# Kernel optimization log

Hardware: AMD Instinct MI355X
Metric: run time of the kernel (lower is better)

Reference implementation:

```python
import jax, jax.numpy as jnp
import numpy as np

N_NODES = 50000
N_EDGES = 819200  # divisible by num_rels=8 -> equal relation segments (implicit rel_ptr)
NUM_RELS = 8
N_HEADS = 4
IN_FEAT = 256
OUT_FEAT = 128
HEAD_DIM = OUT_FEAT // N_HEADS
LEAKY_SLOPE = 0.2


def setup_inputs() -> dict:
    key = jax.random.key(0)
    ks = jax.random.split(key, 7)
    inputs = jax.random.normal(ks[0], (N_NODES, IN_FEAT), dtype=jnp.float32)
    conv_weights = jax.random.normal(ks[1], (NUM_RELS, N_HEADS, IN_FEAT, HEAD_DIM), dtype=jnp.float32) * (1.0 / np.sqrt(IN_FEAT))
    attn_l = jax.random.normal(ks[2], (NUM_RELS, N_HEADS, HEAD_DIM), dtype=jnp.float32) * 0.1
    attn_r = jax.random.normal(ks[3], (NUM_RELS, N_HEADS, HEAD_DIM), dtype=jnp.float32) * 0.1
    h_bias = jax.random.normal(ks[4], (OUT_FEAT,), dtype=jnp.float32) * 0.01
    row_idx = jax.random.randint(ks[5], (N_EDGES,), 0, N_NODES, dtype=jnp.int32)
    col_idx = jax.random.randint(ks[6], (N_EDGES,), 0, N_NODES, dtype=jnp.int32)
    return {
        'inputs': inputs,
        'conv_weights': conv_weights,
        'attn_l': attn_l,
        'attn_r': attn_r,
        'h_bias': h_bias,
        'row_idx': row_idx,
        'col_idx': col_idx,
    }


def reference(inputs, conv_weights, attn_l, attn_r, h_bias, row_idx, col_idx):
    R, H, IN, D = conv_weights.shape
    E = row_idx.shape[0]
    N = inputs.shape[0]
    epr = E // R  # edges per relation (equal segments == rel_ptr)

    # relation-grouped GEMM: per-edge transformed src features [R, epr, H, D]
    src = inputs[row_idx].reshape(R, epr, IN)
    feat_src = jnp.einsum('rei,rhid->rehd', src, conv_weights)
    el = jnp.einsum('rehd,rhd->reh', feat_src, attn_l)

    dst = inputs[col_idx].reshape(R, epr, IN)
    feat_dst = jnp.einsum('rei,rhid->rehd', dst, conv_weights)
    er = jnp.einsum('rehd,rhd->reh', feat_dst, attn_r)

    # fused GAT: leaky_relu(el+er), softmax over incoming edges per dst node
    e = jax.nn.leaky_relu((el + er).reshape(E, H), negative_slope=LEAKY_SLOPE)
    m = jax.ops.segment_max(e, col_idx, num_segments=N)          # [N, H]
    e_exp = jnp.exp(e - m[col_idx])                              # [E, H]
    denom = jax.ops.segment_sum(e_exp, col_idx, num_segments=N)  # [N, H]
    alpha = e_exp / denom[col_idx]                               # [E, H]

    feat = feat_src.reshape(E, H, D)
    h = jax.ops.segment_sum(alpha[:, :, None] * feat, col_idx, num_segments=N)  # [N, H, D]
    h = h.reshape(N, H * D) + h_bias
    # activation=None, self_loop=False, dropout treated as eval (identity)
    return h
```

## Files before the change

### kernel.cpp

```cpp
#include <hip/hip_runtime.h>
#include <hip/hip_bf16.h>

#define N_NODES 50000
#define N_EDGES 819200
#define NUM_RELS 8
#define EPR (N_EDGES / NUM_RELS)
#define N_HEADS 4
#define IN_FEAT 256
#define OUT_FEAT 128
#define HEAD_DIM 32
#define NB_SCAN ((N_NODES + 255) / 256)

typedef __attribute__((ext_vector_type(8))) __bf16 bf16x8;
typedef __attribute__((ext_vector_type(4))) __bf16 bf16x4;
typedef __attribute__((ext_vector_type(4))) float f32x4;

#define SZ_FEAT ((size_t)NUM_RELS * N_NODES * OUT_FEAT)
#define SZ_EL ((size_t)NUM_RELS * N_NODES * N_HEADS)
#define SZ_WB ((size_t)IN_FEAT * 64)
#define SZ_WT ((size_t)NUM_RELS * OUT_FEAT * IN_FEAT / 2)
#define OFF_FEAT ((size_t)0)
#define OFF_EL (OFF_FEAT + SZ_FEAT)
#define OFF_ER (OFF_EL + SZ_EL)
#define OFF_WB (OFF_ER + SZ_EL)
#define OFF_WT (OFF_WB + SZ_WB)
#define OFF_INT (OFF_WT + SZ_WT)
#define IOFF_CNT ((size_t)0)
#define IOFF_PTR ((size_t)N_NODES)
#define IOFF_CUR ((size_t)2 * N_NODES)
#define IOFF_BSUM ((size_t)3 * N_NODES)
#define IOFF_SPAY ((size_t)3 * N_NODES + 256)

__global__ void k_wboth(const float* __restrict__ cw, const float* __restrict__ al,
                        const float* __restrict__ ar, __bf16* __restrict__ wbt) {
    int tid = blockIdx.x * blockDim.x + threadIdx.x;
    if (tid >= IN_FEAT * 64) return;
    int col = tid >> 8, i = tid & 255;
    int side = col >> 5, r = (col >> 2) & 7, h = col & 3;
    const float* av = (side ? ar : al) + (size_t)(r * N_HEADS + h) * HEAD_DIM;
    const float* cwp = cw + ((size_t)(r * N_HEADS + h) * IN_FEAT + i) * HEAD_DIM;
    float s = 0.f;
#pragma unroll
    for (int d = 0; d < HEAD_DIM; ++d) s += cwp[d] * av[d];
    wbt[(size_t)col * IN_FEAT + i] = (__bf16)s;
}

__global__ void k_cvt_w(const float* __restrict__ cw, __bf16* __restrict__ wt) {
    int tid = blockIdx.x * blockDim.x + threadIdx.x;
    if (tid >= NUM_RELS * N_HEADS * IN_FEAT * HEAD_DIM) return;
    int d = tid & 31, k = (tid >> 5) & 255, h = (tid >> 13) & 3, r = tid >> 15;
    float v = cw[tid];
    wt[((size_t)(r * OUT_FEAT + h * HEAD_DIM + d)) * IN_FEAT + k] = (__bf16)v;
}

__global__ __launch_bounds__(256) void k_fused(const float* __restrict__ x,
                                               const __bf16* __restrict__ wt,
                                               const __bf16* __restrict__ wbt,
                                               __bf16* __restrict__ featb,
                                               float* __restrict__ el,
                                               float* __restrict__ er) {
    __shared__ __align__(16) unsigned char sA[65536];
    __shared__ __align__(16) unsigned char sB[16384];
    const int t = threadIdx.x;
    const int lane = t & 63;
    const int w = t >> 6;
    const int wr = w >> 1, wc = w & 1;
    const int n0 = blockIdx.x * 128;

#pragma unroll 8
    for (int i = 0; i < 32; ++i) {
        int flat = i * 256 + t;
        int row = flat >> 6;
        int kq = flat & 63;
        int n = n0 + row;
        if (n >= N_NODES) n = N_NODES - 1;
        float4 v = *(const float4*)(x + (size_t)n * IN_FEAT + kq * 4);
        bf16x4 hv;
        hv[0] = (__bf16)v.x; hv[1] = (__bf16)v.y; hv[2] = (__bf16)v.z; hv[3] = (__bf16)v.w;
        int sg = kq >> 1;
        int slot = (sg & ~7) | ((sg & 7) ^ (row & 7));
        *(bf16x4*)(sA + row * 512 + slot * 16 + (kq & 1) * 8) = hv;
    }
    __syncthreads();

    f32x4 acc[4][4];

    for (int r = 0; r < NUM_RELS; ++r) {
#pragma unroll
        for (int i = 0; i < 4; ++i)
#pragma unroll
            for (int j = 0; j < 4; ++j) acc[i][j] = (f32x4){0.f, 0.f, 0.f, 0.f};
        const __bf16* wtr = wt + (size_t)r * OUT_FEAT * IN_FEAT;

        for (int kc = 0; kc < 4; ++kc) {
#pragma unroll
            for (int i = 0; i < 4; ++i) {
                int flat = i * 256 + t;
                int brow = flat >> 3;
                int s = flat & 7;
                int ssrc = s ^ (brow & 7);
                bf16x8 v = *(const bf16x8*)(wtr + (size_t)brow * IN_FEAT + kc * 64 + ssrc * 8);
                *(bf16x8*)(sB + brow * 128 + s * 16) = v;
            }
            __syncthreads();
#pragma unroll
            for (int ks = 0; ks < 2; ++ks) {
                bf16x8 af[4], bg[4];
#pragma unroll
                for (int rb = 0; rb < 4; ++rb) {
                    int row = wr * 64 + rb * 16 + (lane & 15);
                    int slot = kc * 8 + ((ks * 4 + (lane >> 4)) ^ (row & 7));
                    af[rb] = *(const bf16x8*)(sA + row * 512 + slot * 16);
                }
#pragma unroll
                for (int cb = 0; cb < 4; ++cb) {
                    int brow = wc * 64 + cb * 16 + (lane & 15);
                    int slot = (ks * 4 + (lane >> 4)) ^ (brow & 7);
                    bg[cb] = *(const bf16x8*)(sB + brow * 128 + slot * 16);
                }
#pragma unroll
                for (int rb = 0; rb < 4; ++rb)
#pragma unroll
                    for (int cb = 0; cb < 4; ++cb)
                        acc[rb][cb] = __builtin_amdgcn_mfma_f32_16x16x32_bf16(af[rb], bg[cb], acc[rb][cb], 0, 0, 0);
            }
            __syncthreads();
        }
#pragma unroll
        for (int rb = 0; rb < 4; ++rb) {
#pragma unroll
            for (int q = 0; q < 4; ++q) {
                int row = wr * 64 + rb * 16 + (lane >> 4) * 4 + q;
                int n = n0 + row;
                if (n < N_NODES) {
                    __bf16* fp = featb + ((size_t)r * N_NODES + n) * OUT_FEAT + wc * 64 + (lane & 15);
#pragma unroll
                    for (int cb = 0; cb < 4; ++cb) fp[cb * 16] = (__bf16)acc[rb][cb][q];
                }
            }
        }
    }

#pragma unroll
    for (int i = 0; i < 4; ++i)
#pragma unroll
        for (int j = 0; j < 2; ++j) acc[i][j] = (f32x4){0.f, 0.f, 0.f, 0.f};

    for (int kc = 0; kc < 4; ++kc) {
#pragma unroll
        for (int i = 0; i < 2; ++i) {
            int flat = i * 256 + t;
            int brow = flat >> 3;
            int s = flat & 7;
            int ssrc = s ^ (brow & 7);
            bf16x8 v = *(const bf16x8*)(wbt + (size_t)brow * IN_FEAT + kc * 64 + ssrc * 8);
            *(bf16x8*)(sB + brow * 128 + s * 16) = v;
        }
        __syncthreads();
#pragma unroll
        for (int ks = 0; ks < 2; ++ks) {
            bf16x8 af[4], bg[2];
#pragma unroll
            for (int rb = 0; rb < 4; ++rb) {
                int row = wr * 64 + rb * 16 + (lane & 15);
                int slot = kc * 8 + ((ks * 4 + (lane >> 4)) ^ (row & 7));
                af[rb] = *(const bf16x8*)(sA + row * 512 + slot * 16);
            }
#pragma unroll
            for (int cb = 0; cb < 2; ++cb) {
                int brow = wc * 32 + cb * 16 + (lane & 15);
                int slot = (ks * 4 + (lane >> 4)) ^ (brow & 7);
                bg[cb] = *(const bf16x8*)(sB + brow * 128 + slot * 16);
            }
#pragma unroll
            for (int rb = 0; rb < 4; ++rb)
#pragma unroll
                for (int cb = 0; cb < 2; ++cb)
                    acc[rb][cb] = __builtin_amdgcn_mfma_f32_16x16x32_bf16(af[rb], bg[cb], acc[rb][cb], 0, 0, 0);
        }
        __syncthreads();
    }
#pragma unroll
    for (int rb = 0; rb < 4; ++rb) {
#pragma unroll
        for (int q = 0; q < 4; ++q) {
            int n = n0 + wr * 64 + rb * 16 + (lane >> 4) * 4 + q;
            if (n < N_NODES) {
#pragma unroll
                for (int cb = 0; cb < 2; ++cb) {
                    int c = wc * 32 + cb * 16 + (lane & 15);
                    int side = c >> 5, rr = (c >> 2) & 7, h = c & 3;
                    float* dst = side ? er : el;
                    dst[((size_t)rr * N_NODES + n) * N_HEADS + h] = acc[rb][cb][q];
                }
            }
        }
    }
}

__global__ void k_hist(const int* __restrict__ col, int* __restrict__ cnt) {
    int e = blockIdx.x * blockDim.x + threadIdx.x;
    if (e < N_EDGES) atomicAdd(cnt + col[e], 1);
}

__global__ __launch_bounds__(256) void k_scanA(const int* __restrict__ cnt,
                                               int* __restrict__ excl,
                                               int* __restrict__ bsum) {
    __shared__ int s[256];
    int i = blockIdx.x * 256 + threadIdx.x;
    int v = (i < N_NODES) ? cnt[i] : 0;
    s[threadIdx.x] = v;
    __syncthreads();
#pragma unroll
    for (int off = 1; off < 256; off <<= 1) {
        int t = (threadIdx.x >= off) ? s[threadIdx.x - off] : 0;
        __syncthreads();
        s[threadIdx.x] += t;
        __syncthreads();
    }
    if (i < N_NODES) excl[i] = s[threadIdx.x] - v;
    if (threadIdx.x == 255) bsum[blockIdx.x] = s[255];
}

__global__ __launch_bounds__(256) void k_scanB(int* __restrict__ bsum) {
    __shared__ int s[256];
    int v = (threadIdx.x < NB_SCAN) ? bsum[threadIdx.x] : 0;
    s[threadIdx.x] = v;
    __syncthreads();
#pragma unroll
    for (int off = 1; off < 256; off <<= 1) {
        int t = (threadIdx.x >= off) ? s[threadIdx.x - off] : 0;
        __syncthreads();
        s[threadIdx.x] += t;
        __syncthreads();
    }
    bsum[threadIdx.x] = s[threadIdx.x] - v;
}

__global__ __launch_bounds__(256) void k_scanC(int* __restrict__ ptr,
                                               int* __restrict__ cursor,
                                               const int* __restrict__ bsum) {
    int i = blockIdx.x * 256 + threadIdx.x;
    if (i >= N_NODES) return;
    int p = ptr[i] + bsum[blockIdx.x];
    ptr[i] = p;
    cursor[i] = p;
}

__global__ void k_scatter(const int* __restrict__ row, const int* __restrict__ col,
                          int* __restrict__ cursor, int* __restrict__ spay) {
    int e = blockIdx.x * blockDim.x + threadIdx.x;
    if (e >= N_EDGES) return;
    int c = col[e];
    int pos = atomicAdd(cursor + c, 1);
    spay[pos] = row[e] | ((e / EPR) << 20);
}

__global__ __launch_bounds__(256) void k_agg(const int* __restrict__ ptr,
                                             const int* __restrict__ cnt,
                                             const int* __restrict__ spay,
                                             const float* __restrict__ el,
                                             const float* __restrict__ er,
                                             const __bf16* __restrict__ featb,
                                             const float* __restrict__ bias,
                                             float* __restrict__ out) {
    const int wv = threadIdx.x >> 6, lane = threadIdx.x & 63;
    const int n = blockIdx.x * 4 + wv;
    if (n >= N_NODES) return;
    const int start = ptr[n], len = cnt[n];
    const int h = lane >> 4;
    float accx = 0.f, accy = 0.f, den = 0.f;
    int j = 0;
    for (; j + 4 <= len; j += 4) {
        int p[4];
#pragma unroll
        for (int u = 0; u < 4; ++u) p[u] = spay[start + j + u];
        float w[4], vx[4], vy[4];
#pragma unroll
        for (int u = 0; u < 4; ++u) {
            int rw = p[u] & 0xFFFFF, r = p[u] >> 20;
            size_t rb = (size_t)r * N_NODES;
            float s = el[(rb + rw) * N_HEADS + h] + er[(rb + n) * N_HEADS + h];
            s = s > 0.f ? s : 0.2f * s;
            w[u] = __expf(s);
            ushort2 raw = *(const ushort2*)(featb + (rb + rw) * OUT_FEAT + lane * 2);
            vx[u] = __uint_as_float((unsigned)raw.x << 16);
            vy[u] = __uint_as_float((unsigned)raw.y << 16);
        }
#pragma unroll
        for (int u = 0; u < 4; ++u) {
            accx += w[u] * vx[u];
            accy += w[u] * vy[u];
            den += w[u];
        }
    }
    for (; j < len; ++j) {
        int p = spay[start + j];
        int rw = p & 0xFFFFF, r = p >> 20;
        size_t rb = (size_t)r * N_NODES;
        float s = el[(rb + rw) * N_HEADS + h] + er[(rb + n) * N_HEADS + h];
        s = s > 0.f ? s : 0.2f * s;
        float w = __expf(s);
        ushort2 raw = *(const ushort2*)(featb + (rb + rw) * OUT_FEAT + lane * 2);
        accx += w * __uint_as_float((unsigned)raw.x << 16);
        accy += w * __uint_as_float((unsigned)raw.y << 16);
        den += w;
    }
    float inv = (len > 0) ? 1.f / den : 0.f;
    int o = lane * 2;
    float2 res;
    res.x = accx * inv + bias[o];
    res.y = accy * inv + bias[o + 1];
    *(float2*)(out + (size_t)n * OUT_FEAT + o) = res;
}

extern "C" void kernel_launch(void* const* d_in, const int* in_sizes, int n_in,
                              void* d_out, int out_size, void* d_ws, size_t ws_size,
                              hipStream_t stream) {
    const float* x = (const float*)d_in[0];
    const float* cw = (const float*)d_in[1];
    const float* al = (const float*)d_in[2];
    const float* ar = (const float*)d_in[3];
    const float* bias = (const float*)d_in[4];
    const int* row = (const int*)d_in[5];
    const int* col = (const int*)d_in[6];
    float* out = (float*)d_out;
    float* ws = (float*)d_ws;

    __bf16* featb = (__bf16*)(ws + OFF_FEAT);
    float* el = ws + OFF_EL;
    float* er = ws + OFF_ER;
    __bf16* wbt = (__bf16*)(ws + OFF_WB);
    __bf16* wt = (__bf16*)(ws + OFF_WT);
    int* iw = (int*)(ws + OFF_INT);
    int* cnt = iw + IOFF_CNT;
    int* ptr = iw + IOFF_PTR;
    int* cur = iw + IOFF_CUR;
    int* bsum = iw + IOFF_BSUM;
    int* spay = iw + IOFF_SPAY;

    hipMemsetAsync(cnt, 0, N_NODES * sizeof(int), stream);

    k_wboth<<<(IN_FEAT * 64 + 255) / 256, 256, 0, stream>>>(cw, al, ar, wbt);
    k_cvt_w<<<(NUM_RELS * N_HEADS * IN_FEAT * HEAD_DIM + 255) / 256, 256, 0, stream>>>(cw, wt);
    k_fused<<<(N_NODES + 127) / 128, 256, 0, stream>>>(x, wt, wbt, featb, el, er);

    k_hist<<<(N_EDGES + 255) / 256, 256, 0, stream>>>(col, cnt);
    k_scanA<<<NB_SCAN, 256, 0, stream>>>(cnt, ptr, bsum);
    k_scanB<<<1, 256, 0, stream>>>(bsum);
    k_scanC<<<NB_SCAN, 256, 0, stream>>>(ptr, cur, bsum);
    k_scatter<<<(N_EDGES + 255) / 256, 256, 0, stream>>>(row, col, cur, spay);

    k_agg<<<(N_NODES + 3) / 4, 256, 0, stream>>>(ptr, cnt, spay, el, er, featb, bias, out);
}
```

Measured before the change: 213.4 us.

## Split wavefront into two half-waves processing alternate edges with 8-byte loads

The aggregation kernel now has each half of a 64-lane wavefront handle alternate incoming edges. Each lane loads four bf16 features (8 bytes) instead of two, and the two halves are combined with a cross-lane shuffle at the end. The per-relation er values for the destination node are preloaded into registers, so the loop no longer reloads them for every edge. This aims to double the number of independent gathers in flight per wave and widen each load, at the cost of predicated tail handling, an extra register array and a reduction step.

New measurement: 238.7 us. 1.12x slower.

```diff
diff --git a/kernel.cpp b/kernel.cpp
--- a/kernel.cpp
+++ b/kernel.cpp
@@ -268,50 +268,49 @@
     const int n = blockIdx.x * 4 + wv;
     if (n >= N_NODES) return;
     const int start = ptr[n], len = cnt[n];
-    const int h = lane >> 4;
-    float accx = 0.f, accy = 0.f, den = 0.f;
-    int j = 0;
-    for (; j + 4 <= len; j += 4) {
-        int p[4];
-#pragma unroll
-        for (int u = 0; u < 4; ++u) p[u] = spay[start + j + u];
-        float w[4], vx[4], vy[4];
-#pragma unroll
-        for (int u = 0; u < 4; ++u) {
-            int rw = p[u] & 0xFFFFF, r = p[u] >> 20;
-            size_t rb = (size_t)r * N_NODES;
-            float s = el[(rb + rw) * N_HEADS + h] + er[(rb + n) * N_HEADS + h];
-            s = s > 0.f ? s : 0.2f * s;
-            w[u] = __expf(s);
-            ushort2 raw = *(const ushort2*)(featb + (rb + rw) * OUT_FEAT + lane * 2);
-            vx[u] = __uint_as_float((unsigned)raw.x << 16);
-            vy[u] = __uint_as_float((unsigned)raw.y << 16);
-        }
-#pragma unroll
-        for (int u = 0; u < 4; ++u) {
-            accx += w[u] * vx[u];
-            accy += w[u] * vy[u];
-            den += w[u];
-        }
-    }
-    for (; j < len; ++j) {
-        int p = spay[start + j];
+    const int half = lane >> 5;
+    const int hl = lane & 31;
+    const int o0 = hl * 4;
+    const int h = o0 >> 5;
+
+    float er_r[8];
+#pragma unroll
+    for (int r = 0; r < 8; ++r)
+        er_r[r] = er[((size_t)r * N_NODES + n) * N_HEADS + h];
+
+    float a0 = 0.f, a1 = 0.f, a2 = 0.f, a3 = 0.f, den = 0.f;
+    const int nit = (len + 1) >> 1;
+#pragma unroll 2
+    for (int j = 0; j < nit; ++j) {
+        int idx = 2 * j + half;
+        bool valid = idx < len;
+        int p = valid ? spay[start + idx] : 0;
         int rw = p & 0xFFFFF, r = p >> 20;
         size_t rb = (size_t)r * N_NODES;
-        float s = el[(rb + rw) * N_HEADS + h] + er[(rb + n) * N_HEADS + h];
+        float s = el[(rb + rw) * N_HEADS + h] + er_r[r];
         s = s > 0.f ? s : 0.2f * s;
-        float w = __expf(s);
-        ushort2 raw = *(const ushort2*)(featb + (rb + rw) * OUT_FEAT + lane * 2);
-        accx += w * __uint_as_float((unsigned)raw.x << 16);
-        accy += w * __uint_as_float((unsigned)raw.y << 16);
-        den += w;
-    }
-    float inv = (len > 0) ? 1.f / den : 0.f;
-    int o = lane * 2;
-    float2 res;
-    res.x = accx * inv + bias[o];
-    res.y = accy * inv + bias[o + 1];
-    *(float2*)(out + (size_t)n * OUT_FEAT + o) = res;
+        float wgt = valid ? __expf(s) : 0.f;
+        ushort4 raw = *(const ushort4*)(featb + (rb + rw) * OUT_FEAT + o0);
+        a0 += wgt * __uint_as_float((unsigned)raw.x << 16);
+        a1 += wgt * __uint_as_float((unsigned)raw.y << 16);
+        a2 += wgt * __uint_as_float((unsigned)raw.z << 16);
+        a3 += wgt * __uint_as_float((unsigned)raw.w << 16);
+        den += wgt;
+    }
+    a0 += __shfl_down(a0, 32);
+    a1 += __shfl_down(a1, 32);
+    a2 += __shfl_down(a2, 32);
+    a3 += __shfl_down(a3, 32);
+    den += __shfl_down(den, 32);
+    if (half == 0) {
+        float inv = (len > 0) ? 1.f / den : 0.f;
+        float4 res;
+        res.x = a0 * inv + bias[o0];
+        res.y = a1 * inv + bias[o0 + 1];
+        res.z = a2 * inv + bias[o0 + 2];
+        res.w = a3 * inv + bias[o0 + 3];
+        *(float4*)(out + (size_t)n * OUT_FEAT + o0) = res;
+    }
 }
 
 extern "C" void kernel_launch(void* const* d_in, const int* in_sizes, int n_in,
```
